# Optimization experiments

Measured on AMD Instinct MI355X. Metric: run time of the kernel, lower is better.

Reference implementation:

```python
import jax, jax.numpy as jnp
import numpy as np

N = 30000      # num nodes
E = 600000     # num edges
D = 128        # feature dim (all layers)
R = 7          # num_relation
G = 16         # num graphs in batch
L = 3          # num layers (hidden_dims = [128,128,128])


def setup_inputs() -> dict:
    key = jax.random.key(0)
    ks = jax.random.split(key, 10)
    x = jax.random.normal(ks[0], (N, D), dtype=jnp.float32)
    node_in = jax.random.randint(ks[1], (E,), 0, N)
    node_out = jax.random.randint(ks[2], (E,), 0, N)
    relation = jax.random.randint(ks[3], (E,), 0, R)
    edge_weight = jax.random.uniform(ks[4], (E,), dtype=jnp.float32)
    node2graph = jnp.sort(jax.random.randint(ks[5], (N,), 0, G))
    # learned params: per-layer relational linear (R*D -> D) and self-loop linear (D -> D)
    Wr = jax.random.normal(ks[6], (L, R * D, D), dtype=jnp.float32) * 0.02
    br = jnp.zeros((L, D), dtype=jnp.float32)
    Wl = jax.random.normal(ks[7], (L, D, D), dtype=jnp.float32) * 0.02
    bl = jnp.zeros((L, D), dtype=jnp.float32)
    return dict(x=x, node_in=node_in, node_out=node_out, relation=relation,
                edge_weight=edge_weight, node2graph=node2graph,
                Wr=Wr, br=br, Wl=Wl, bl=bl)


def reference(x, node_in, node_out, relation, edge_weight, node2graph, Wr, br, Wl, bl):
    # relation-indexed destination segment: node_out * R + relation
    seg = node_out * R + relation            # (E,)
    ew = edge_weight[:, None]                # (E, 1)
    h = x
    for i in range(L):
        msg = h[node_in] * ew                                         # gather + weight, (E, D)
        upd = jax.ops.segment_sum(msg, seg, num_segments=N * R)       # scatter_add, (N*R, D)
        upd = upd.reshape(N, R * D)                                   # per-relation concat
        h = jax.nn.relu(upd @ Wr[i] + br[i] + h @ Wl[i] + bl[i])      # linear + self-loop + act
    node_feature = h                                                  # (N, D)
    graph_feature = jax.ops.segment_sum(node_feature, node2graph, num_segments=G)  # sum readout
    return graph_feature, node_feature
```

## Files before the change

kernel.cpp:

```cpp
#include <hip/hip_runtime.h>
#include <hip/hip_bf16.h>

#define NN 30000
#define NE 600000
#define DD 128
#define RR 7
#define GG 16
#define LL 3

#define NB64 ((NN + 63) / 64)

typedef short bf16x8 __attribute__((ext_vector_type(8)));
typedef float f32x4  __attribute__((ext_vector_type(4)));

__device__ __forceinline__ unsigned short f2bf(float f) {
    unsigned u = __float_as_uint(f);
    unsigned r = (u + 0x7fffu + ((u >> 16) & 1u)) >> 16;
    return (unsigned short)r;
}
__device__ __forceinline__ float bf2f(unsigned short b) {
    return __uint_as_float(((unsigned)b) << 16);
}
__device__ __forceinline__ ushort2 pk2bf(float a, float b) {
    __hip_bfloat162 t = __float22bfloat162_rn(make_float2(a, b));
    return *(ushort2*)&t;
}

__device__ __forceinline__ void gl_lds16(const void* g, void* l) {
    __builtin_amdgcn_global_load_lds(
        (const __attribute__((address_space(1))) void*)g,
        (__attribute__((address_space(3))) void*)l, 16, 0, 0);
}

__global__ __launch_bounds__(256) void pack_weights(
    const float* __restrict__ Wl,
    const float* __restrict__ Wr,
    unsigned short* __restrict__ Bw)
{
    int t = blockIdx.x * 256 + threadIdx.x;
    if (t >= LL * 1024 * DD) return;
    int l = t >> 17;
    int rem = t & 131071;
    int n = rem >> 7;
    int k = rem & 127;
    float v;
    if (n < DD) {
        v = Wl[(size_t)l * DD * DD + k * DD + n];
    } else {
        int q = n - DD;
        v = Wr[(size_t)l * RR * DD * DD + (size_t)((q >> 7) * DD + k) * DD + (q & 127)];
    }
    Bw[(size_t)l * 1024 * DD + n * DD + k] = f2bf(v);
}

__global__ __launch_bounds__(256) void convert_bf16(
    const float* __restrict__ in, unsigned short* __restrict__ out, int n4)
{
    int i = blockIdx.x * 256 + threadIdx.x;
    if (i >= n4) return;
    float4 v = ((const float4*)in)[i];
    ushort2 lo = pk2bf(v.x, v.y);
    ushort2 hi = pk2bf(v.z, v.w);
    ((ushort4*)out)[i] = make_ushort4(lo.x, lo.y, hi.x, hi.y);
}

__global__ __launch_bounds__(256) void bucket_hist(
    const int* __restrict__ node_out, int* __restrict__ bcnt, int E)
{
    int e = blockIdx.x * 256 + threadIdx.x;
    if (e < E) atomicAdd(&bcnt[(node_out[e] >> 6) * 16], 1);
}

__global__ __launch_bounds__(512) void bucket_scan(
    const int* __restrict__ bcnt, int* __restrict__ bstart,
    int* __restrict__ bcur, int nb)
{
    __shared__ int s[512];
    int t = threadIdx.x;
    int v = (t < nb) ? bcnt[t * 16] : 0;
    s[t] = v;
    __syncthreads();
#pragma unroll
    for (int off = 1; off < 512; off <<= 1) {
        int u = (t >= off) ? s[t - off] : 0;
        __syncthreads();
        s[t] += u;
        __syncthreads();
    }
    if (t <= nb) {
        int excl = s[t] - v;
        bstart[t] = excl;
        if (t < nb) bcur[t * 16] = excl;
    }
}

__global__ __launch_bounds__(256) void bucket_scatter(
    const int* __restrict__ node_in,
    const int* __restrict__ node_out,
    const int* __restrict__ relation,
    const float* __restrict__ ew,
    int* __restrict__ bcur,
    int2* __restrict__ tmp,
    int E)
{
    int e = blockIdx.x * 256 + threadIdx.x;
    if (e >= E) return;
    int o = node_out[e];
    int pos = atomicAdd(&bcur[(o >> 6) * 16], 1);
    tmp[pos] = make_int2(((o & 63) << 18) | (node_in[e] << 3) | relation[e],
                         __float_as_int(ew[e]));
}

__global__ __launch_bounds__(256) void bucket_sort(
    const int2* __restrict__ tmp,
    const int* __restrict__ bstart,
    int2* __restrict__ meta,
    int* __restrict__ start,
    int N)
{
    __shared__ int hist[64];
    __shared__ int scan[64];
    __shared__ int cur[64];
    const int b = blockIdx.x;
    const int t = threadIdx.x;
    const int s0 = bstart[b];
    const int s1 = bstart[b + 1];

    if (t < 64) hist[t] = 0;
    __syncthreads();
    for (int i = s0 + t; i < s1; i += 256)
        atomicAdd(&hist[((unsigned)tmp[i].x) >> 18], 1);
    __syncthreads();

    int v = (t < 64) ? hist[t] : 0;
    if (t < 64) scan[t] = v;
    __syncthreads();
#pragma unroll
    for (int off = 1; off < 64; off <<= 1) {
        int u = (t < 64 && t >= off) ? scan[t - off] : 0;
        __syncthreads();
        if (t < 64) scan[t] += u;
        __syncthreads();
    }
    if (t < 64) {
        int excl = scan[t] - v;
        cur[t] = s0 + excl;
        int node = b * 64 + t;
        if (node <= N) start[node] = s0 + excl;
    }
    __syncthreads();

    for (int i = s0 + t; i < s1; i += 256) {
        int2 m = tmp[i];
        int j = ((unsigned)m.x) >> 18;
        int pos = atomicAdd(&cur[j], 1);
        int key = m.x & 0x3ffff;
        int in = key >> 3, rel = key & 7;
        meta[pos] = make_int2((in * RR + rel) << 7, m.y);
    }
}

__global__ __launch_bounds__(256) void gemm_mfma(
    const unsigned short* __restrict__ hb,
    const unsigned short* __restrict__ Bw,
    const float* __restrict__ br,
    const float* __restrict__ bl,
    unsigned short* __restrict__ haccb,
    unsigned short* __restrict__ Zb,
    int N)
{
    __shared__ unsigned short As[64 * 128];
    __shared__ unsigned short Bs[256 * 128];

    const int tid  = threadIdx.x;
    const int wave = tid >> 6;
    const int lane = tid & 63;
    const int quad = lane >> 4;
    const int l16  = lane & 15;
    const int row0 = blockIdx.x * 64;
    const int col0 = blockIdx.y * 256;

    const int lr = lane >> 4;
    const int ls = lane & 15;

#pragma unroll
    for (int i = 0; i < 4; ++i) {
        int g = i * 4 + wave;
        int r = g * 4 + lr;
        int slot = ls ^ (r & 7);
        gl_lds16(hb + (size_t)(row0 + r) * 128 + slot * 8, As + g * 512);
    }
#pragma unroll
    for (int i = 0; i < 16; ++i) {
        int g = i * 4 + wave;
        int r = g * 4 + lr;
        int slot = ls ^ (r & 7);
        gl_lds16(Bw + (size_t)(col0 + r) * 128 + slot * 8, Bs + g * 512);
    }
    __syncthreads();

    f32x4 acc[4][4];
#pragma unroll
    for (int mt = 0; mt < 4; ++mt)
#pragma unroll
        for (int nt = 0; nt < 4; ++nt)
            acc[mt][nt] = (f32x4){0.f, 0.f, 0.f, 0.f};

    const unsigned short* As_l = As + l16 * 128;
    const unsigned short* Bs_l = Bs + (wave * 64 + l16) * 128;
    const int swz = l16 & 7;

#pragma unroll
    for (int kc = 0; kc < 4; ++kc) {
        int so = ((kc * 4 + quad) ^ swz) * 8;
        bf16x8 a0 = *(const bf16x8*)(As_l + 0 * 16 * 128 + so);
        bf16x8 a1 = *(const bf16x8*)(As_l + 1 * 16 * 128 + so);
        bf16x8 a2 = *(const bf16x8*)(As_l + 2 * 16 * 128 + so);
        bf16x8 a3 = *(const bf16x8*)(As_l + 3 * 16 * 128 + so);
        bf16x8 b0 = *(const bf16x8*)(Bs_l + 0 * 16 * 128 + so);
        bf16x8 b1 = *(const bf16x8*)(Bs_l + 1 * 16 * 128 + so);
        bf16x8 b2 = *(const bf16x8*)(Bs_l + 2 * 16 * 128 + so);
        bf16x8 b3 = *(const bf16x8*)(Bs_l + 3 * 16 * 128 + so);
#pragma unroll
        for (int mt = 0; mt < 4; ++mt) {
            bf16x8 a = (mt == 0) ? a0 : (mt == 1) ? a1 : (mt == 2) ? a2 : a3;
            acc[mt][0] = __builtin_amdgcn_mfma_f32_16x16x32_bf16(a, b0, acc[mt][0], 0, 0, 0);
            acc[mt][1] = __builtin_amdgcn_mfma_f32_16x16x32_bf16(a, b1, acc[mt][1], 0, 0, 0);
            acc[mt][2] = __builtin_amdgcn_mfma_f32_16x16x32_bf16(a, b2, acc[mt][2], 0, 0, 0);
            acc[mt][3] = __builtin_amdgcn_mfma_f32_16x16x32_bf16(a, b3, acc[mt][3], 0, 0, 0);
        }
    }

    if (col0 == 0 && wave < 2) {
        float bias[4];
#pragma unroll
        for (int nt = 0; nt < 4; ++nt) {
            int c = wave * 64 + nt * 16 + l16;
            bias[nt] = br[c] + bl[c];
        }
#pragma unroll
        for (int mt = 0; mt < 4; ++mt) {
#pragma unroll
            for (int reg = 0; reg < 4; ++reg) {
                int row = row0 + mt * 16 + quad * 4 + reg;
                if (row < N) {
                    ushort2 p01 = pk2bf(acc[mt][0][reg] + bias[0],
                                        acc[mt][1][reg] + bias[1]);
                    ushort2 p23 = pk2bf(acc[mt][2][reg] + bias[2],
                                        acc[mt][3][reg] + bias[3]);
                    unsigned short* dst = haccb + (size_t)row * 128 + wave * 64 + l16;
                    dst[0]  = p01.x;
                    dst[16] = p01.y;
                    dst[32] = p23.x;
                    dst[48] = p23.y;
                }
            }
        }
    } else {
        const int zc = col0 + wave * 64 - 128;
#pragma unroll
        for (int mt = 0; mt < 4; ++mt) {
#pragma unroll
            for (int reg = 0; reg < 4; ++reg) {
                int row = row0 + mt * 16 + quad * 4 + reg;
                if (row < N) {
                    ushort2 p01 = pk2bf(acc[mt][0][reg], acc[mt][1][reg]);
                    ushort2 p23 = pk2bf(acc[mt][2][reg], acc[mt][3][reg]);
                    unsigned short* dst = Zb + (size_t)row * (RR * DD) + zc + l16;
                    dst[0]  = p01.x;
                    dst[16] = p01.y;
                    dst[32] = p23.x;
                    dst[48] = p23.y;
                }
            }
        }
    }
}

__global__ __launch_bounds__(256) void aggregate(
    const unsigned short* __restrict__ Zb,
    const int* __restrict__ start,
    const int2* __restrict__ meta,
    const unsigned short* __restrict__ haccb,
    float* __restrict__ out_f32,
    unsigned short* __restrict__ out_bf16,
    int N)
{
    int wid = (blockIdx.x * 256 + threadIdx.x) >> 6;
    int lane = threadIdx.x & 63;
    if (wid >= N) return;

    int e0 = start[wid];
    int e1 = start[wid + 1];

    float accx = 0.f, accy = 0.f;
    int e = e0;
    for (; e + 8 <= e1; e += 8) {
        unsigned u[8]; float wt[8];
#pragma unroll
        for (int j = 0; j < 8; ++j) {
            int2 m = meta[e + j];
            u[j] = *(const unsigned*)(Zb + m.x + lane * 2);
            wt[j] = __int_as_float(m.y);
        }
#pragma unroll
        for (int j = 0; j < 8; ++j) {
            accx = fmaf(wt[j], __uint_as_float(u[j] << 16), accx);
            accy = fmaf(wt[j], __uint_as_float(u[j] & 0xffff0000u), accy);
        }
    }
    for (; e + 2 <= e1; e += 2) {
        int2 m0 = meta[e];
        int2 m1 = meta[e + 1];
        unsigned u0 = *(const unsigned*)(Zb + m0.x + lane * 2);
        unsigned u1 = *(const unsigned*)(Zb + m1.x + lane * 2);
        float w0 = __int_as_float(m0.y), w1 = __int_as_float(m1.y);
        accx = fmaf(w0, __uint_as_float(u0 << 16), accx);
        accy = fmaf(w0, __uint_as_float(u0 & 0xffff0000u), accy);
        accx = fmaf(w1, __uint_as_float(u1 << 16), accx);
        accy = fmaf(w1, __uint_as_float(u1 & 0xffff0000u), accy);
    }
    if (e < e1) {
        int2 m = meta[e];
        unsigned u = *(const unsigned*)(Zb + m.x + lane * 2);
        float wt = __int_as_float(m.y);
        accx = fmaf(wt, __uint_as_float(u << 16), accx);
        accy = fmaf(wt, __uint_as_float(u & 0xffff0000u), accy);
    }

    unsigned bu = *(const unsigned*)(haccb + (size_t)wid * DD + lane * 2);
    float ox = fmaxf(bf2f((unsigned short)(bu & 0xffffu)) + accx, 0.f);
    float oy = fmaxf(bf2f((unsigned short)(bu >> 16)) + accy, 0.f);
    if (out_f32) {
        *(float2*)(out_f32 + (size_t)wid * DD + lane * 2) = make_float2(ox, oy);
    }
    if (out_bf16) {
        ushort2 o = pk2bf(ox, oy);
        *(ushort2*)(out_bf16 + (size_t)wid * DD + lane * 2) = o;
    }
}

__global__ __launch_bounds__(256) void graph_sum(
    const float* __restrict__ nf,
    const int* __restrict__ n2g,
    float* __restrict__ gf,
    int N)
{
    int t = blockIdx.x * 256 + threadIdx.x;
    int chunk = t >> 5;
    int lane = t & 31;
    int n0 = chunk * 16;
    if (n0 >= N) return;
    int nend = n0 + 16; if (nend > N) nend = N;

    float4 acc = make_float4(0.f, 0.f, 0.f, 0.f);
    int curg = n2g[n0];
    for (int n = n0; n < nend; ++n) {
        int g = n2g[n];
        if (g != curg) {
            float* dst = gf + (size_t)curg * DD + lane * 4;
            atomicAdd(dst + 0, acc.x); atomicAdd(dst + 1, acc.y);
            atomicAdd(dst + 2, acc.z); atomicAdd(dst + 3, acc.w);
            acc = make_float4(0.f, 0.f, 0.f, 0.f);
            curg = g;
        }
        float4 v = *(const float4*)(nf + (size_t)n * DD + lane * 4);
        acc.x += v.x; acc.y += v.y; acc.z += v.z; acc.w += v.w;
    }
    float* dst = gf + (size_t)curg * DD + lane * 4;
    atomicAdd(dst + 0, acc.x); atomicAdd(dst + 1, acc.y);
    atomicAdd(dst + 2, acc.z); atomicAdd(dst + 3, acc.w);
}

extern "C" void kernel_launch(void* const* d_in, const int* in_sizes, int n_in,
                              void* d_out, int out_size, void* d_ws, size_t ws_size,
                              hipStream_t stream)
{
    const float* x        = (const float*)d_in[0];
    const int*   node_in  = (const int*)d_in[1];
    const int*   node_out = (const int*)d_in[2];
    const int*   relation = (const int*)d_in[3];
    const float* ew       = (const float*)d_in[4];
    const int*   n2g      = (const int*)d_in[5];
    const float* Wr       = (const float*)d_in[6];
    const float* br       = (const float*)d_in[7];
    const float* Wl       = (const float*)d_in[8];
    const float* bl       = (const float*)d_in[9];

    float* out = (float*)d_out;
    float* gf = out;
    float* nf = out + GG * DD;

    char* w = (char*)d_ws;
    unsigned short* Zb   = (unsigned short*)w; w += (size_t)NN * RR * DD * 2;
    unsigned short* haccb= (unsigned short*)w; w += (size_t)NN * DD * 2;
    unsigned short* hbA  = (unsigned short*)w; w += (size_t)NN * DD * 2;
    unsigned short* hbB  = (unsigned short*)w; w += (size_t)NN * DD * 2;
    unsigned short* Bw   = (unsigned short*)w; w += (size_t)LL * 1024 * DD * 2;
    int2*  meta   = (int2*)w;                  w += (size_t)NE * 8;
    int2*  tmp    = (int2*)w;                  w += (size_t)NE * 8;
    int*   start  = (int*)w;                   w += (size_t)(NN + 1) * 4 + 60;
    int*   bcnt   = (int*)w;                   w += (size_t)NB64 * 16 * 4 + 64;
    int*   bcur   = (int*)w;                   w += (size_t)NB64 * 16 * 4 + 64;
    int*   bstart = (int*)w;                   w += (size_t)(NB64 + 1) * 4 + 60;

    const int N = NN, E = NE;

    pack_weights<<<(LL * 1024 * DD + 255) / 256, 256, 0, stream>>>(Wl, Wr, Bw);
    convert_bf16<<<(N * DD / 4 + 255) / 256, 256, 0, stream>>>(x, hbA, N * DD / 4);

    hipMemsetAsync(bcnt, 0, (size_t)NB64 * 16 * sizeof(int), stream);
    bucket_hist<<<(E + 255) / 256, 256, 0, stream>>>(node_out, bcnt, E);
    bucket_scan<<<1, 512, 0, stream>>>(bcnt, bstart, bcur, NB64);
    bucket_scatter<<<(E + 255) / 256, 256, 0, stream>>>(
        node_in, node_out, relation, ew, bcur, tmp, E);
    bucket_sort<<<NB64, 256, 0, stream>>>(tmp, bstart, meta, start, N);

    dim3 ggrid((N + 63) / 64, 4);
    unsigned short* hin = hbA;
    unsigned short* hnext = hbB;
    for (int l = 0; l < LL; ++l) {
        const float* br_l = br + (size_t)l * DD;
        const float* bl_l = bl + (size_t)l * DD;
        const unsigned short* Bw_l = Bw + (size_t)l * 1024 * DD;

        gemm_mfma<<<ggrid, 256, 0, stream>>>(hin, Bw_l, br_l, bl_l, haccb, Zb, N);

        bool last = (l == LL - 1);
        aggregate<<<(N * 64 + 255) / 256, 256, 0, stream>>>(
            Zb, start, meta, haccb,
            last ? nf : (float*)nullptr,
            last ? (unsigned short*)nullptr : hnext, N);

        unsigned short* t = hin; hin = hnext; hnext = t;
    }

    hipMemsetAsync(gf, 0, (size_t)GG * DD * sizeof(float), stream);
    int chunks = (N + 15) / 16;
    graph_sum<<<(chunks * 32 + 255) / 256, 256, 0, stream>>>(nf, n2g, gf, N);
}
```

Baseline: 329.5 us.

## Split aggregate wave into four 16-lane groups with 16-byte gathers and shuffled metadata

The aggregate kernel now has each wavefront process four edges at once. Each 16-lane group loads a full 256-byte bf16 row using uint4 loads, and the partial sums are combined with cross-group shuffles at the end. Edge metadata is loaded coalesced, 64 entries at a time, and broadcast with shuffles instead of being loaded per lane per edge. This is meant to raise memory-level parallelism and reduce load instruction count. The cost is extra shuffle work and some wasted lanes when the edge count is not a multiple of four.

```diff
diff --git a/kernel.cpp b/kernel.cpp
--- a/kernel.cpp
+++ b/kernel.cpp
@@ -290,53 +290,72 @@
     int lane = threadIdx.x & 63;
     if (wid >= N) return;
 
+    const int grp  = lane >> 4;
+    const int l16  = lane & 15;
+    const int base = l16 * 8;
+
     int e0 = start[wid];
     int e1 = start[wid + 1];
 
-    float accx = 0.f, accy = 0.f;
-    int e = e0;
-    for (; e + 8 <= e1; e += 8) {
-        unsigned u[8]; float wt[8];
-#pragma unroll
-        for (int j = 0; j < 8; ++j) {
-            int2 m = meta[e + j];
-            u[j] = *(const unsigned*)(Zb + m.x + lane * 2);
-            wt[j] = __int_as_float(m.y);
-        }
-#pragma unroll
-        for (int j = 0; j < 8; ++j) {
-            accx = fmaf(wt[j], __uint_as_float(u[j] << 16), accx);
-            accy = fmaf(wt[j], __uint_as_float(u[j] & 0xffff0000u), accy);
-        }
-    }
-    for (; e + 2 <= e1; e += 2) {
-        int2 m0 = meta[e];
-        int2 m1 = meta[e + 1];
-        unsigned u0 = *(const unsigned*)(Zb + m0.x + lane * 2);
-        unsigned u1 = *(const unsigned*)(Zb + m1.x + lane * 2);
-        float w0 = __int_as_float(m0.y), w1 = __int_as_float(m1.y);
-        accx = fmaf(w0, __uint_as_float(u0 << 16), accx);
-        accy = fmaf(w0, __uint_as_float(u0 & 0xffff0000u), accy);
-        accx = fmaf(w1, __uint_as_float(u1 << 16), accx);
-        accy = fmaf(w1, __uint_as_float(u1 & 0xffff0000u), accy);
-    }
-    if (e < e1) {
-        int2 m = meta[e];
-        unsigned u = *(const unsigned*)(Zb + m.x + lane * 2);
-        float wt = __int_as_float(m.y);
-        accx = fmaf(wt, __uint_as_float(u << 16), accx);
-        accy = fmaf(wt, __uint_as_float(u & 0xffff0000u), accy);
-    }
-
-    unsigned bu = *(const unsigned*)(haccb + (size_t)wid * DD + lane * 2);
-    float ox = fmaxf(bf2f((unsigned short)(bu & 0xffffu)) + accx, 0.f);
-    float oy = fmaxf(bf2f((unsigned short)(bu >> 16)) + accy, 0.f);
-    if (out_f32) {
-        *(float2*)(out_f32 + (size_t)wid * DD + lane * 2) = make_float2(ox, oy);
-    }
-    if (out_bf16) {
-        ushort2 o = pk2bf(ox, oy);
-        *(ushort2*)(out_bf16 + (size_t)wid * DD + lane * 2) = o;
+    float acc[8];
+#pragma unroll
+    for (int k = 0; k < 8; ++k) acc[k] = 0.f;
+
+    for (int eb = e0; eb < e1; eb += 64) {
+        int2 mm = make_int2(0, 0);
+        if (eb + lane < e1) mm = meta[eb + lane];
+        int cnt = e1 - eb; if (cnt > 64) cnt = 64;
+        for (int j = 0; j < cnt; j += 4) {
+            int idx = j + grp;
+            int key = __shfl(mm.x, idx, 64);
+            float wt = __uint_as_float((unsigned)__shfl(mm.y, idx, 64));
+            uint4 u = *(const uint4*)(Zb + (size_t)(unsigned)key + base);
+            acc[0] = fmaf(wt, __uint_as_float(u.x << 16),          acc[0]);
+            acc[1] = fmaf(wt, __uint_as_float(u.x & 0xffff0000u),  acc[1]);
+            acc[2] = fmaf(wt, __uint_as_float(u.y << 16),          acc[2]);
+            acc[3] = fmaf(wt, __uint_as_float(u.y & 0xffff0000u),  acc[3]);
+            acc[4] = fmaf(wt, __uint_as_float(u.z << 16),          acc[4]);
+            acc[5] = fmaf(wt, __uint_as_float(u.z & 0xffff0000u),  acc[5]);
+            acc[6] = fmaf(wt, __uint_as_float(u.w << 16),          acc[6]);
+            acc[7] = fmaf(wt, __uint_as_float(u.w & 0xffff0000u),  acc[7]);
+        }
+    }
+
+#pragma unroll
+    for (int k = 0; k < 8; ++k) {
+        acc[k] += __shfl_xor(acc[k], 16, 64);
+        acc[k] += __shfl_xor(acc[k], 32, 64);
+    }
+
+    uint4 hb4 = *(const uint4*)(haccb + (size_t)wid * DD + base);
+    float o[8];
+    o[0] = fmaxf(__uint_as_float(hb4.x << 16)         + acc[0], 0.f);
+    o[1] = fmaxf(__uint_as_float(hb4.x & 0xffff0000u) + acc[1], 0.f);
+    o[2] = fmaxf(__uint_as_float(hb4.y << 16)         + acc[2], 0.f);
+    o[3] = fmaxf(__uint_as_float(hb4.y & 0xffff0000u) + acc[3], 0.f);
+    o[4] = fmaxf(__uint_as_float(hb4.z << 16)         + acc[4], 0.f);
+    o[5] = fmaxf(__uint_as_float(hb4.z & 0xffff0000u) + acc[5], 0.f);
+    o[6] = fmaxf(__uint_as_float(hb4.w << 16)         + acc[6], 0.f);
+    o[7] = fmaxf(__uint_as_float(hb4.w & 0xffff0000u) + acc[7], 0.f);
+
+    if (grp == 0) {
+        if (out_f32) {
+            float* dst = out_f32 + (size_t)wid * DD + base;
+            *(float4*)(dst)     = make_float4(o[0], o[1], o[2], o[3]);
+            *(float4*)(dst + 4) = make_float4(o[4], o[5], o[6], o[7]);
+        }
+        if (out_bf16) {
+            ushort2 p0 = pk2bf(o[0], o[1]);
+            ushort2 p1 = pk2bf(o[2], o[3]);
+            ushort2 p2 = pk2bf(o[4], o[5]);
+            ushort2 p3 = pk2bf(o[6], o[7]);
+            uint4 ub;
+            ub.x = (unsigned)p0.x | ((unsigned)p0.y << 16);
+            ub.y = (unsigned)p1.x | ((unsigned)p1.y << 16);
+            ub.z = (unsigned)p2.x | ((unsigned)p2.y << 16);
+            ub.w = (unsigned)p3.x | ((unsigned)p3.y << 16);
+            *(uint4*)(out_bf16 + (size_t)wid * DD + base) = ub;
+        }
     }
 }
 
```

Measured after the change: 329.5 us. Within noise of the previous version (+0.0%).
